# Kernel optimization log

Hardware: AMD Instinct MI355X
Metric: run time of the kernel (lower is better)

Reference implementation:

```python
import jax, jax.numpy as jnp
import numpy as np

D_MODEL = 1024
NUM_HEADS = 16
D_K = D_MODEL // NUM_HEADS
BATCH = 2
SEQ = 2048


def setup_inputs() -> dict:
    key = jax.random.key(0)
    ks = jax.random.split(key, 9)
    s = 1.0 / np.sqrt(D_MODEL)
    X = jax.random.normal(ks[0], (BATCH, SEQ, D_MODEL), dtype=jnp.float32)
    # causal mask, broadcastable over batch and heads; 0 means masked
    mask = jnp.tril(jnp.ones((SEQ, SEQ), dtype=jnp.int32))[None, None]
    W_Q = jax.random.uniform(ks[1], (D_MODEL, D_MODEL), jnp.float32, -s, s)
    b_Q = jax.random.uniform(ks[2], (D_MODEL,), jnp.float32, -s, s)
    W_K = jax.random.uniform(ks[3], (D_MODEL, D_MODEL), jnp.float32, -s, s)
    b_K = jax.random.uniform(ks[4], (D_MODEL,), jnp.float32, -s, s)
    W_V = jax.random.uniform(ks[5], (D_MODEL, D_MODEL), jnp.float32, -s, s)
    b_V = jax.random.uniform(ks[6], (D_MODEL,), jnp.float32, -s, s)
    W_O = jax.random.uniform(ks[7], (D_MODEL, D_MODEL), jnp.float32, -s, s)
    b_O = jax.random.uniform(ks[8], (D_MODEL,), jnp.float32, -s, s)
    return {"X": X, "mask": mask, "W_Q": W_Q, "b_Q": b_Q, "W_K": W_K,
            "b_K": b_K, "W_V": W_V, "b_V": b_V, "W_O": W_O, "b_O": b_O}


def reference(X, mask, W_Q, b_Q, W_K, b_K, W_V, b_V, W_O, b_O):
    B, S, _ = X.shape
    H, Dk = NUM_HEADS, D_K
    # projections; torch Linear uses y = x @ W.T + b; here W_* is stored as [in, out]
    Q = (X @ W_Q + b_Q).reshape(B, S, H, Dk).transpose(0, 2, 1, 3)  # [B,H,S,Dk]
    K = (X @ W_K + b_K).reshape(B, S, H, Dk).transpose(0, 2, 1, 3)
    V = (X @ W_V + b_V).reshape(B, S, H, Dk).transpose(0, 2, 1, 3)
    scores = jnp.einsum("bhqd,bhkd->bhqk", Q, K) / jnp.sqrt(jnp.asarray(Dk, X.dtype))
    scores = jnp.where(mask == 0, -jnp.inf, scores)
    attn = jax.nn.softmax(scores, axis=-1)  # [B,H,S,S]
    out = jnp.einsum("bhqk,bhkd->bhqd", attn, V)
    out = out.transpose(0, 2, 1, 3).reshape(B, S, H * Dk)
    return out @ W_O + b_O
```

## Files before the change

### kernel.cpp

```cpp
#include <hip/hip_runtime.h>
#include <math.h>

#define S_LEN 2048
#define DM 1024
#define NH 16
#define DK 64
#define BB 2
#define MROWS (BB * S_LEN)
#define QTILES (S_LEN / 64)
#define LOG2E 1.44269504088896340736f

typedef __attribute__((ext_vector_type(8))) short bf16x8;
typedef __attribute__((ext_vector_type(4))) float f32x4;

__device__ __forceinline__ unsigned short f2bf(float f) {
    unsigned int u = __builtin_bit_cast(unsigned int, f);
    u += 0x7fff + ((u >> 16) & 1);
    return (unsigned short)(u >> 16);
}

__device__ __forceinline__ float hw_exp2(float x) {
    return __builtin_amdgcn_exp2f(x);
}

__device__ __forceinline__ void gload_lds16(const unsigned short* g, unsigned short* l) {
    __builtin_amdgcn_global_load_lds(
        (const __attribute__((address_space(1))) unsigned int*)(const void*)g,
        (__attribute__((address_space(3))) unsigned int*)(void*)l, 16, 0, 0);
}

__global__ __launch_bounds__(256) void convert_bf16_kernel(
    const float* __restrict__ in, unsigned short* __restrict__ out, int n) {
    int i = (blockIdx.x * 256 + threadIdx.x) * 4;
    if (i + 3 < n) {
        float4 v = *(const float4*)(in + i);
        ushort4 o;
        o.x = f2bf(v.x); o.y = f2bf(v.y); o.z = f2bf(v.z); o.w = f2bf(v.w);
        *(ushort4*)(out + i) = o;
    }
}

__global__ __launch_bounds__(256) void transpose_bf16_kernel(
    const float* __restrict__ in, unsigned short* __restrict__ out,
    int rows, int cols) {
    __shared__ float tile[32][33];
    const int tx = threadIdx.x & 31, ty = threadIdx.x >> 5;
    const int c = blockIdx.x * 32 + tx;
    for (int i = 0; i < 32; i += 8)
        tile[ty + i][tx] = in[(size_t)(blockIdx.y * 32 + ty + i) * cols + c];
    __syncthreads();
    const int oc = blockIdx.y * 32 + tx;
    for (int i = 0; i < 32; i += 8)
        out[(size_t)(blockIdx.x * 32 + ty + i) * rows + oc] = f2bf(tile[tx][ty + i]);
}

__global__ __launch_bounds__(256) void gemm_bf16_kernel(
    const unsigned short* __restrict__ A,
    const unsigned short* __restrict__ Bt,
    const float* __restrict__ bQ, const float* __restrict__ bK,
    const float* __restrict__ bV,
    unsigned short* __restrict__ outQ, unsigned short* __restrict__ outK,
    unsigned short* __restrict__ outV,
    float* __restrict__ out_f,
    int K, int mode) {
    __shared__ __align__(16) unsigned short smem[4 * 64 * 72];
    const int tid = threadIdx.x;
    const int wave = tid >> 6, lane = tid & 63;
    const int lq = lane >> 4, ln = lane & 15;
    const int m0 = blockIdx.y * 128, n0 = blockIdx.x * 128;
    const int wr = (wave >> 1) * 64, wc = (wave & 1) * 64;

    f32x4 acc[4][4];
#pragma unroll
    for (int i = 0; i < 4; ++i)
#pragma unroll
        for (int j = 0; j < 4; ++j)
            acc[i][j] = (f32x4){0.f, 0.f, 0.f, 0.f};

    const unsigned short* ga = A  + (size_t)(m0 + (tid >> 2)) * K + (tid & 3) * 8;
    const unsigned short* gb = Bt + (size_t)(n0 + (tid >> 2)) * K + (tid & 3) * 8;
    const size_t half = (size_t)64 * K;

    {
        unsigned short* An = smem;
        unsigned short* Bn = smem + 4096;
        gload_lds16(ga, An + tid * 8);
        gload_lds16(ga + half, An + 2048 + tid * 8);
        gload_lds16(gb, Bn + tid * 8);
        gload_lds16(gb + half, Bn + 2048 + tid * 8);
    }

    for (int k0 = 0; k0 < K; k0 += 32) {
        const int cur = (k0 >> 5) & 1;
        unsigned short* As = smem + cur * 8192;
        unsigned short* Bs = As + 4096;
        __syncthreads();
        if (k0 + 32 < K) {
            unsigned short* An = smem + (cur ^ 1) * 8192;
            unsigned short* Bn = An + 4096;
            gload_lds16(ga + k0 + 32, An + tid * 8);
            gload_lds16(ga + half + k0 + 32, An + 2048 + tid * 8);
            gload_lds16(gb + k0 + 32, Bn + tid * 8);
            gload_lds16(gb + half + k0 + 32, Bn + 2048 + tid * 8);
        }
        bf16x8 af[4], bfv[4];
#pragma unroll
        for (int i = 0; i < 4; ++i) af[i]  = *(const bf16x8*)&As[(wr + i * 16 + ln) * 32 + lq * 8];
#pragma unroll
        for (int j = 0; j < 4; ++j) bfv[j] = *(const bf16x8*)&Bs[(wc + j * 16 + ln) * 32 + lq * 8];
#pragma unroll
        for (int i = 0; i < 4; ++i)
#pragma unroll
            for (int j = 0; j < 4; ++j)
                acc[i][j] = __builtin_amdgcn_mfma_f32_16x16x32_bf16(af[i], bfv[j], acc[i][j], 0, 0, 0);
    }
    __syncthreads();

    if (mode == 0) {
        const int which = n0 >> 10;
        const float* bias = which == 0 ? bQ : (which == 1 ? bK : bV);
        const float scale = which == 0 ? 0.125f * LOG2E : 1.0f;
        unsigned short* ob = which == 0 ? outQ : (which == 1 ? outK : outV);
        unsigned short* Ts = &smem[wave * 64 * 72];
#pragma unroll
        for (int i = 0; i < 4; ++i)
#pragma unroll
            for (int j = 0; j < 4; ++j)
#pragma unroll
                for (int r = 0; r < 4; ++r) {
                    int rl = i * 16 + lq * 4 + r;
                    int cl = j * 16 + ln;
                    float v = (acc[i][j][r] + bias[(n0 & 1023) + wc + cl]) * scale;
                    if (which == 2) Ts[cl * 72 + rl] = f2bf(v);
                    else            Ts[rl * 72 + cl] = f2bf(v);
                }
        const int hh = ((n0 & 1023) + wc) >> 6;
        const int bI = (m0 + wr) >> 11, sbase = (m0 + wr) & 2047;
        if (which <= 1) {
            unsigned short* dst = ob + ((size_t)(bI * NH + hh) * S_LEN + sbase) * DK;
#pragma unroll
            for (int t = 0; t < 8; ++t) {
                int rl = t * 8 + (lane >> 3);
                *(uint4*)(dst + rl * DK + (lane & 7) * 8) =
                    *(const uint4*)&Ts[rl * 72 + (lane & 7) * 8];
            }
        } else {
            unsigned short* dst = ob + ((size_t)(bI * NH + hh) * DK) * S_LEN + sbase;
#pragma unroll
            for (int t = 0; t < 8; ++t) {
                int dkl = t * 8 + (lane >> 3);
                *(uint4*)(dst + (size_t)dkl * S_LEN + (lane & 7) * 8) =
                    *(const uint4*)&Ts[dkl * 72 + (lane & 7) * 8];
            }
        }
    } else {
#pragma unroll
        for (int i = 0; i < 4; ++i)
#pragma unroll
            for (int j = 0; j < 4; ++j)
#pragma unroll
                for (int r = 0; r < 4; ++r) {
                    int m = m0 + wr + i * 16 + lq * 4 + r;
                    int n = n0 + wc + j * 16 + ln;
                    out_f[(size_t)m * DM + n] = acc[i][j][r] + bQ[n];
                }
    }
}

__global__ __launch_bounds__(256, 2) void attn_kernel(
    const unsigned short* __restrict__ Qg,
    const unsigned short* __restrict__ Kg,
    const unsigned short* __restrict__ Vg,
    unsigned short* __restrict__ Og) {
    __shared__ __align__(16) unsigned short KBUF[2 * 128 * 64];
    __shared__ __align__(16) unsigned short VBUF[2 * 64 * 128];
    __shared__ __align__(16) unsigned short Pw[4][16 * 40];

    const int tid = threadIdx.x;
    const int wave = tid >> 6, lane = tid & 63;
    const int lq = lane >> 4, ln = lane & 15;
    const int bh = blockIdx.y, b = bh >> 4, h = bh & 15;
    const int bx = blockIdx.x;
    const int qtA = QTILES - 1 - bx, qtB = bx;
    const int nkvA = (qtA + 2) >> 1;
    const int nkvB = (qtB + 2) >> 1;
    const int T = nkvA + nkvB;

    const unsigned short* Qb = Qg + (size_t)bh * S_LEN * DK;
    const unsigned short* Kb = Kg + (size_t)bh * S_LEN * DK;
    const unsigned short* Vb = Vg + (size_t)bh * DK * S_LEN;

    const int krow_l = lane >> 3;
    const int kchunk = (lane & 7) ^ krow_l;
    const int vrow_l = lane >> 4;

    {
#pragma unroll
        for (int s = 0; s < 4; ++s)
            gload_lds16(Kb + (size_t)(wave * 32 + s * 8 + krow_l) * DK + kchunk * 8,
                        KBUF + (wave * 32 + s * 8) * 64 + lane * 8);
#pragma unroll
        for (int s = 0; s < 4; ++s) {
            int rv = wave * 16 + s * 4 + vrow_l;
            int c  = (lane & 15) ^ (s * 4 + vrow_l);
            gload_lds16(Vb + (size_t)rv * S_LEN + c * 8,
                        VBUF + (wave * 16 + s * 4) * 128 + lane * 8);
        }
    }

    int q0 = qtA * 64;
    const int qrowoff = wave * 16 + ln;
    bf16x8 qf0 = *(const bf16x8*)(Qb + (q0 + qrowoff) * DK + lq * 8);
    bf16x8 qf1 = *(const bf16x8*)(Qb + (q0 + qrowoff) * DK + 32 + lq * 8);

    f32x4 oacc[4];
#pragma unroll
    for (int i = 0; i < 4; ++i) oacc[i] = (f32x4){0.f, 0.f, 0.f, 0.f};
    float m0r = -INFINITY, m1r = -INFINITY, m2r = -INFINITY, m3r = -INFINITY;
    float l0r = 0.f, l1r = 0.f, l2r = 0.f, l3r = 0.f;

    for (int g = 0; g < T; ++g) {
        const int cur = g & 1;
        unsigned short* Kl = KBUF + cur * 8192;
        unsigned short* Vl = VBUF + cur * 8192;
        __syncthreads();

        if (g + 1 < T) {
            const int kv0n = (g + 1 < nkvA ? g + 1 : g + 1 - nkvA) * 128;
            unsigned short* Kn = KBUF + (cur ^ 1) * 8192;
            unsigned short* Vn = VBUF + (cur ^ 1) * 8192;
#pragma unroll
            for (int s = 0; s < 4; ++s)
                gload_lds16(Kb + (size_t)(kv0n + wave * 32 + s * 8 + krow_l) * DK + kchunk * 8,
                            Kn + (wave * 32 + s * 8) * 64 + lane * 8);
#pragma unroll
            for (int s = 0; s < 4; ++s) {
                int rv = wave * 16 + s * 4 + vrow_l;
                int c  = (lane & 15) ^ (s * 4 + vrow_l);
                gload_lds16(Vb + (size_t)rv * S_LEN + kv0n + c * 8,
                            Vn + (wave * 16 + s * 4) * 128 + lane * 8);
            }
        }

        const int kv0 = (g < nkvA ? g : g - nkvA) * 128;
        const bool lastOfSeg = (g == nkvA - 1) || (g == T - 1);

        f32x4 sc[8];
#pragma unroll
        for (int ct = 0; ct < 8; ++ct) {
            const int rbase = (ct * 16 + ln) * 64;
            bf16x8 k0 = *(const bf16x8*)&Kl[rbase + ((lq ^ (ln & 7)) * 8)];
            bf16x8 k1 = *(const bf16x8*)&Kl[rbase + (((lq + 4) ^ (ln & 7)) * 8)];
            f32x4 a = (f32x4){0.f, 0.f, 0.f, 0.f};
            a = __builtin_amdgcn_mfma_f32_16x16x32_bf16(qf0, k0, a, 0, 0, 0);
            a = __builtin_amdgcn_mfma_f32_16x16x32_bf16(qf1, k1, a, 0, 0, 0);
            sc[ct] = a;
        }

        if (lastOfSeg) {
#pragma unroll
            for (int ct = 0; ct < 8; ++ct) {
                int col = kv0 + ct * 16 + ln;
#pragma unroll
                for (int r = 0; r < 4; ++r) {
                    int row = q0 + wave * 16 + lq * 4 + r;
                    if (col > row) sc[ct][r] = -INFINITY;
                }
            }
        }

#pragma unroll
        for (int r = 0; r < 4; ++r) {
            float mx = fmaxf(fmaxf(fmaxf(sc[0][r], sc[1][r]), fmaxf(sc[2][r], sc[3][r])),
                             fmaxf(fmaxf(sc[4][r], sc[5][r]), fmaxf(sc[6][r], sc[7][r])));
#pragma unroll
            for (int off = 1; off < 16; off <<= 1)
                mx = fmaxf(mx, __shfl_xor(mx, off));
            float mold = r == 0 ? m0r : (r == 1 ? m1r : (r == 2 ? m2r : m3r));
            float mnew = fmaxf(mold, mx);
            float alpha = hw_exp2(mold - mnew);
#pragma unroll
            for (int dkt = 0; dkt < 4; ++dkt) oacc[dkt][r] *= alpha;
            float rs = 0.f;
#pragma unroll
            for (int ct = 0; ct < 8; ++ct) {
                float pv = hw_exp2(sc[ct][r] - mnew);
                sc[ct][r] = pv;
                rs += pv;
            }
#pragma unroll
            for (int off = 1; off < 16; off <<= 1)
                rs += __shfl_xor(rs, off);
            if (r == 0) { l0r = l0r * alpha + rs; m0r = mnew; }
            else if (r == 1) { l1r = l1r * alpha + rs; m1r = mnew; }
            else if (r == 2) { l2r = l2r * alpha + rs; m2r = mnew; }
            else { l3r = l3r * alpha + rs; m3r = mnew; }
        }

        unsigned short* Pp = Pw[wave];
#pragma unroll
        for (int qd = 0; qd < 4; ++qd) {
#pragma unroll
            for (int c2 = 0; c2 < 2; ++c2)
#pragma unroll
                for (int r = 0; r < 4; ++r)
                    Pp[(lq * 4 + r) * 40 + c2 * 16 + ln] = f2bf(sc[qd * 2 + c2][r]);
            bf16x8 pf = *(const bf16x8*)&Pp[ln * 40 + lq * 8];
#pragma unroll
            for (int dkt = 0; dkt < 4; ++dkt) {
                const unsigned short* vr =
                    &Vl[(dkt * 16 + ln) * 128 + (((qd * 4 + lq) ^ ln) * 8)];
                oacc[dkt] = __builtin_amdgcn_mfma_f32_16x16x32_bf16(pf, *(const bf16x8*)vr, oacc[dkt], 0, 0, 0);
            }
        }

        if (g == nkvA - 1) {
#pragma unroll
            for (int r = 0; r < 4; ++r) {
                float lr = r == 0 ? l0r : (r == 1 ? l1r : (r == 2 ? l2r : l3r));
                float inv = 1.0f / lr;
                int s = q0 + wave * 16 + lq * 4 + r;
#pragma unroll
                for (int dkt = 0; dkt < 4; ++dkt)
                    Og[((size_t)(b * S_LEN + s)) * DM + h * 64 + dkt * 16 + ln] =
                        f2bf(oacc[dkt][r] * inv);
            }
            q0 = qtB * 64;
            qf0 = *(const bf16x8*)(Qb + (q0 + qrowoff) * DK + lq * 8);
            qf1 = *(const bf16x8*)(Qb + (q0 + qrowoff) * DK + 32 + lq * 8);
#pragma unroll
            for (int i = 0; i < 4; ++i) oacc[i] = (f32x4){0.f, 0.f, 0.f, 0.f};
            m0r = m1r = m2r = m3r = -INFINITY;
            l0r = l1r = l2r = l3r = 0.f;
        }
    }

#pragma unroll
    for (int r = 0; r < 4; ++r) {
        float lr = r == 0 ? l0r : (r == 1 ? l1r : (r == 2 ? l2r : l3r));
        float inv = 1.0f / lr;
        int s = q0 + wave * 16 + lq * 4 + r;
#pragma unroll
        for (int dkt = 0; dkt < 4; ++dkt)
            Og[((size_t)(b * S_LEN + s)) * DM + h * 64 + dkt * 16 + ln] =
                f2bf(oacc[dkt][r] * inv);
    }
}

extern "C" void kernel_launch(void* const* d_in, const int* in_sizes, int n_in,
                              void* d_out, int out_size, void* d_ws, size_t ws_size,
                              hipStream_t stream) {
    const float* X   = (const float*)d_in[0];
    const float* W_Q = (const float*)d_in[2];
    const float* b_Q = (const float*)d_in[3];
    const float* W_K = (const float*)d_in[4];
    const float* b_K = (const float*)d_in[5];
    const float* W_V = (const float*)d_in[6];
    const float* b_V = (const float*)d_in[7];
    const float* W_O = (const float*)d_in[8];
    const float* b_O = (const float*)d_in[9];

    unsigned short* Xb    = (unsigned short*)d_ws;
    unsigned short* WqkvT = Xb    + (size_t)MROWS * DM;
    unsigned short* WoT   = WqkvT + (size_t)3 * DM * DM;
    unsigned short* Qb    = WoT   + (size_t)DM * DM;
    unsigned short* Kb    = Qb    + (size_t)MROWS * DM;
    unsigned short* Vtb   = Kb    + (size_t)MROWS * DM;
    unsigned short* Ob    = Vtb   + (size_t)MROWS * DM;

    convert_bf16_kernel<<<(MROWS * DM) / 1024, 256, 0, stream>>>(X, Xb, MROWS * DM);
    dim3 tg(DM / 32, DM / 32);
    transpose_bf16_kernel<<<tg, 256, 0, stream>>>(W_Q, WqkvT, DM, DM);
    transpose_bf16_kernel<<<tg, 256, 0, stream>>>(W_K, WqkvT + (size_t)DM * DM, DM, DM);
    transpose_bf16_kernel<<<tg, 256, 0, stream>>>(W_V, WqkvT + (size_t)2 * DM * DM, DM, DM);
    transpose_bf16_kernel<<<tg, 256, 0, stream>>>(W_O, WoT, DM, DM);

    gemm_bf16_kernel<<<dim3(3 * DM / 128, MROWS / 128), 256, 0, stream>>>(
        Xb, WqkvT, b_Q, b_K, b_V, Qb, Kb, Vtb, nullptr, DM, 0);

    attn_kernel<<<dim3(QTILES / 2, BB * NH), 256, 0, stream>>>(Qb, Kb, Vtb, Ob);

    gemm_bf16_kernel<<<dim3(DM / 128, MROWS / 128), 256, 0, stream>>>(
        Ob, WoT, b_O, nullptr, nullptr, nullptr, nullptr, nullptr, (float*)d_out, DM, 1);
}
```

Before: 226.9 us.

## Merge prep kernels, add narrower O-projection GEMM, compute softmax row sums via MFMA

```diff
diff --git a/kernel.cpp b/kernel.cpp
--- a/kernel.cpp
+++ b/kernel.cpp
@@ -29,40 +29,45 @@
         (__attribute__((address_space(3))) unsigned int*)(void*)l, 16, 0, 0);
 }
 
-__global__ __launch_bounds__(256) void convert_bf16_kernel(
-    const float* __restrict__ in, unsigned short* __restrict__ out, int n) {
-    int i = (blockIdx.x * 256 + threadIdx.x) * 4;
-    if (i + 3 < n) {
-        float4 v = *(const float4*)(in + i);
+__global__ __launch_bounds__(256) void prep_kernel(
+    const float* __restrict__ X, unsigned short* __restrict__ Xb,
+    const float* __restrict__ W_Q, const float* __restrict__ W_K,
+    const float* __restrict__ W_V, const float* __restrict__ W_O,
+    unsigned short* __restrict__ WqkvT, unsigned short* __restrict__ WoT) {
+    const int z = blockIdx.z;
+    if (z == 0) {
+        int i = (blockIdx.x * 256 + threadIdx.x) * 4;
+        float4 v = *(const float4*)(X + i);
         ushort4 o;
         o.x = f2bf(v.x); o.y = f2bf(v.y); o.z = f2bf(v.z); o.w = f2bf(v.w);
-        *(ushort4*)(out + i) = o;
-    }
-}
-
-__global__ __launch_bounds__(256) void transpose_bf16_kernel(
-    const float* __restrict__ in, unsigned short* __restrict__ out,
-    int rows, int cols) {
+        *(ushort4*)(Xb + i) = o;
+        return;
+    }
+    if (blockIdx.x >= (DM / 32) * (DM / 32)) return;
+    const float* in = z == 1 ? W_Q : (z == 2 ? W_K : (z == 3 ? W_V : W_O));
+    unsigned short* out = z == 4 ? WoT : (WqkvT + (size_t)(z - 1) * DM * DM);
     __shared__ float tile[32][33];
+    const int bx = blockIdx.x & 31, by = blockIdx.x >> 5;
     const int tx = threadIdx.x & 31, ty = threadIdx.x >> 5;
-    const int c = blockIdx.x * 32 + tx;
+    const int c = bx * 32 + tx;
+#pragma unroll
     for (int i = 0; i < 32; i += 8)
-        tile[ty + i][tx] = in[(size_t)(blockIdx.y * 32 + ty + i) * cols + c];
+        tile[ty + i][tx] = in[(size_t)(by * 32 + ty + i) * DM + c];
     __syncthreads();
-    const int oc = blockIdx.y * 32 + tx;
+    const int oc = by * 32 + tx;
+#pragma unroll
     for (int i = 0; i < 32; i += 8)
-        out[(size_t)(blockIdx.x * 32 + ty + i) * rows + oc] = f2bf(tile[tx][ty + i]);
-}
-
-__global__ __launch_bounds__(256) void gemm_bf16_kernel(
+        out[(size_t)(bx * 32 + ty + i) * DM + oc] = f2bf(tile[tx][ty + i]);
+}
+
+__global__ __launch_bounds__(256) void gemm_qkv_kernel(
     const unsigned short* __restrict__ A,
     const unsigned short* __restrict__ Bt,
     const float* __restrict__ bQ, const float* __restrict__ bK,
     const float* __restrict__ bV,
     unsigned short* __restrict__ outQ, unsigned short* __restrict__ outK,
-    unsigned short* __restrict__ outV,
-    float* __restrict__ out_f,
-    int K, int mode) {
+    unsigned short* __restrict__ outV) {
+    const int K = DM;
     __shared__ __align__(16) unsigned short smem[4 * 64 * 72];
     const int tid = threadIdx.x;
     const int wave = tid >> 6, lane = tid & 63;
@@ -116,55 +121,108 @@
     }
     __syncthreads();
 
-    if (mode == 0) {
-        const int which = n0 >> 10;
-        const float* bias = which == 0 ? bQ : (which == 1 ? bK : bV);
-        const float scale = which == 0 ? 0.125f * LOG2E : 1.0f;
-        unsigned short* ob = which == 0 ? outQ : (which == 1 ? outK : outV);
-        unsigned short* Ts = &smem[wave * 64 * 72];
+    const int which = n0 >> 10;
+    const float* bias = which == 0 ? bQ : (which == 1 ? bK : bV);
+    const float scale = which == 0 ? 0.125f * LOG2E : 1.0f;
+    unsigned short* ob = which == 0 ? outQ : (which == 1 ? outK : outV);
+    unsigned short* Ts = &smem[wave * 64 * 72];
+#pragma unroll
+    for (int i = 0; i < 4; ++i)
+#pragma unroll
+        for (int j = 0; j < 4; ++j)
+#pragma unroll
+            for (int r = 0; r < 4; ++r) {
+                int rl = i * 16 + lq * 4 + r;
+                int cl = j * 16 + ln;
+                float v = (acc[i][j][r] + bias[(n0 & 1023) + wc + cl]) * scale;
+                if (which == 2) Ts[cl * 72 + rl] = f2bf(v);
+                else            Ts[rl * 72 + cl] = f2bf(v);
+            }
+    const int hh = ((n0 & 1023) + wc) >> 6;
+    const int bI = (m0 + wr) >> 11, sbase = (m0 + wr) & 2047;
+    if (which <= 1) {
+        unsigned short* dst = ob + ((size_t)(bI * NH + hh) * S_LEN + sbase) * DK;
+#pragma unroll
+        for (int t = 0; t < 8; ++t) {
+            int rl = t * 8 + (lane >> 3);
+            *(uint4*)(dst + rl * DK + (lane & 7) * 8) =
+                *(const uint4*)&Ts[rl * 72 + (lane & 7) * 8];
+        }
+    } else {
+        unsigned short* dst = ob + ((size_t)(bI * NH + hh) * DK) * S_LEN + sbase;
+#pragma unroll
+        for (int t = 0; t < 8; ++t) {
+            int dkl = t * 8 + (lane >> 3);
+            *(uint4*)(dst + (size_t)dkl * S_LEN + (lane & 7) * 8) =
+                *(const uint4*)&Ts[dkl * 72 + (lane & 7) * 8];
+        }
+    }
+}
+
+__global__ __launch_bounds__(256) void gemm_o_kernel(
+    const unsigned short* __restrict__ A,
+    const unsigned short* __restrict__ Bt,
+    const float* __restrict__ bias,
+    float* __restrict__ out_f) {
+    const int K = DM;
+    __shared__ __align__(16) unsigned short smem[2 * 6144];
+    const int tid = threadIdx.x;
+    const int wave = tid >> 6, lane = tid & 63;
+    const int lq = lane >> 4, ln = lane & 15;
+    const int m0 = blockIdx.y * 128, n0 = blockIdx.x * 64;
+    const int wr = (wave >> 1) * 64, wc = (wave & 1) * 32;
+
+    f32x4 acc[4][2];
+#pragma unroll
+    for (int i = 0; i < 4; ++i)
+#pragma unroll
+        for (int j = 0; j < 2; ++j)
+            acc[i][j] = (f32x4){0.f, 0.f, 0.f, 0.f};
+
+    const unsigned short* ga = A  + (size_t)(m0 + (tid >> 2)) * K + (tid & 3) * 8;
+    const unsigned short* gb = Bt + (size_t)(n0 + (tid >> 2)) * K + (tid & 3) * 8;
+    const size_t half = (size_t)64 * K;
+
+    {
+        unsigned short* An = smem;
+        gload_lds16(ga, An + tid * 8);
+        gload_lds16(ga + half, An + 2048 + tid * 8);
+        gload_lds16(gb, An + 4096 + tid * 8);
+    }
+
+    for (int k0 = 0; k0 < K; k0 += 32) {
+        const int cur = (k0 >> 5) & 1;
+        unsigned short* As = smem + cur * 6144;
+        unsigned short* Bs = As + 4096;
+        __syncthreads();
+        if (k0 + 32 < K) {
+            unsigned short* An = smem + (cur ^ 1) * 6144;
+            gload_lds16(ga + k0 + 32, An + tid * 8);
+            gload_lds16(ga + half + k0 + 32, An + 2048 + tid * 8);
+            gload_lds16(gb + k0 + 32, An + 4096 + tid * 8);
+        }
+        bf16x8 af[4], bfv[2];
+#pragma unroll
+        for (int i = 0; i < 4; ++i) af[i]  = *(const bf16x8*)&As[(wr + i * 16 + ln) * 32 + lq * 8];
+#pragma unroll
+        for (int j = 0; j < 2; ++j) bfv[j] = *(const bf16x8*)&Bs[(wc + j * 16 + ln) * 32 + lq * 8];
 #pragma unroll
         for (int i = 0; i < 4; ++i)
 #pragma unroll
-            for (int j = 0; j < 4; ++j)
-#pragma unroll
-                for (int r = 0; r < 4; ++r) {
-                    int rl = i * 16 + lq * 4 + r;
-                    int cl = j * 16 + ln;
-                    float v = (acc[i][j][r] + bias[(n0 & 1023) + wc + cl]) * scale;
-                    if (which == 2) Ts[cl * 72 + rl] = f2bf(v);
-                    else            Ts[rl * 72 + cl] = f2bf(v);
-                }
-        const int hh = ((n0 & 1023) + wc) >> 6;
-        const int bI = (m0 + wr) >> 11, sbase = (m0 + wr) & 2047;
-        if (which <= 1) {
-            unsigned short* dst = ob + ((size_t)(bI * NH + hh) * S_LEN + sbase) * DK;
-#pragma unroll
-            for (int t = 0; t < 8; ++t) {
-                int rl = t * 8 + (lane >> 3);
-                *(uint4*)(dst + rl * DK + (lane & 7) * 8) =
-                    *(const uint4*)&Ts[rl * 72 + (lane & 7) * 8];
-            }
-        } else {
-            unsigned short* dst = ob + ((size_t)(bI * NH + hh) * DK) * S_LEN + sbase;
-#pragma unroll
-            for (int t = 0; t < 8; ++t) {
-                int dkl = t * 8 + (lane >> 3);
-                *(uint4*)(dst + (size_t)dkl * S_LEN + (lane & 7) * 8) =
-                    *(const uint4*)&Ts[dkl * 72 + (lane & 7) * 8];
-            }
-        }
-    } else {
-#pragma unroll
-        for (int i = 0; i < 4; ++i)
-#pragma unroll
-            for (int j = 0; j < 4; ++j)
-#pragma unroll
-                for (int r = 0; r < 4; ++r) {
-                    int m = m0 + wr + i * 16 + lq * 4 + r;
-                    int n = n0 + wc + j * 16 + ln;
-                    out_f[(size_t)m * DM + n] = acc[i][j][r] + bQ[n];
-                }
-    }
+            for (int j = 0; j < 2; ++j)
+                acc[i][j] = __builtin_amdgcn_mfma_f32_16x16x32_bf16(af[i], bfv[j], acc[i][j], 0, 0, 0);
+    }
+
+#pragma unroll
+    for (int i = 0; i < 4; ++i)
+#pragma unroll
+        for (int j = 0; j < 2; ++j)
+#pragma unroll
+            for (int r = 0; r < 4; ++r) {
+                int m = m0 + wr + i * 16 + lq * 4 + r;
+                int n = n0 + wc + j * 16 + ln;
+                out_f[(size_t)m * DM + n] = acc[i][j][r] + bias[n];
+            }
 }
 
 __global__ __launch_bounds__(256, 2) void attn_kernel(
@@ -213,11 +271,15 @@
     bf16x8 qf0 = *(const bf16x8*)(Qb + (q0 + qrowoff) * DK + lq * 8);
     bf16x8 qf1 = *(const bf16x8*)(Qb + (q0 + qrowoff) * DK + 32 + lq * 8);
 
+    const short one_bf = (short)0x3F80;
+    const bf16x8 onesf = {one_bf, one_bf, one_bf, one_bf,
+                          one_bf, one_bf, one_bf, one_bf};
+
     f32x4 oacc[4];
+    f32x4 lacc = (f32x4){0.f, 0.f, 0.f, 0.f};
 #pragma unroll
     for (int i = 0; i < 4; ++i) oacc[i] = (f32x4){0.f, 0.f, 0.f, 0.f};
     float m0r = -INFINITY, m1r = -INFINITY, m2r = -INFINITY, m3r = -INFINITY;
-    float l0r = 0.f, l1r = 0.f, l2r = 0.f, l3r = 0.f;
 
     for (int g = 0; g < T; ++g) {
         const int cur = g & 1;
@@ -281,20 +343,14 @@
             float alpha = hw_exp2(mold - mnew);
 #pragma unroll
             for (int dkt = 0; dkt < 4; ++dkt) oacc[dkt][r] *= alpha;
-            float rs = 0.f;
-#pragma unroll
-            for (int ct = 0; ct < 8; ++ct) {
-                float pv = hw_exp2(sc[ct][r] - mnew);
-                sc[ct][r] = pv;
-                rs += pv;
-            }
-#pragma unroll
-            for (int off = 1; off < 16; off <<= 1)
-                rs += __shfl_xor(rs, off);
-            if (r == 0) { l0r = l0r * alpha + rs; m0r = mnew; }
-            else if (r == 1) { l1r = l1r * alpha + rs; m1r = mnew; }
-            else if (r == 2) { l2r = l2r * alpha + rs; m2r = mnew; }
-            else { l3r = l3r * alpha + rs; m3r = mnew; }
+            lacc[r] *= alpha;
+#pragma unroll
+            for (int ct = 0; ct < 8; ++ct)
+                sc[ct][r] = hw_exp2(sc[ct][r] - mnew);
+            if (r == 0) m0r = mnew;
+            else if (r == 1) m1r = mnew;
+            else if (r == 2) m2r = mnew;
+            else m3r = mnew;
         }
 
         unsigned short* Pp = Pw[wave];
@@ -306,6 +362,7 @@
                 for (int r = 0; r < 4; ++r)
                     Pp[(lq * 4 + r) * 40 + c2 * 16 + ln] = f2bf(sc[qd * 2 + c2][r]);
             bf16x8 pf = *(const bf16x8*)&Pp[ln * 40 + lq * 8];
+            lacc = __builtin_amdgcn_mfma_f32_16x16x32_bf16(pf, onesf, lacc, 0, 0, 0);
 #pragma unroll
             for (int dkt = 0; dkt < 4; ++dkt) {
                 const unsigned short* vr =
@@ -317,8 +374,7 @@
         if (g == nkvA - 1) {
 #pragma unroll
             for (int r = 0; r < 4; ++r) {
-                float lr = r == 0 ? l0r : (r == 1 ? l1r : (r == 2 ? l2r : l3r));
-                float inv = 1.0f / lr;
+                float inv = 1.0f / lacc[r];
                 int s = q0 + wave * 16 + lq * 4 + r;
 #pragma unroll
                 for (int dkt = 0; dkt < 4; ++dkt)
@@ -330,15 +386,14 @@
             qf1 = *(const bf16x8*)(Qb + (q0 + qrowoff) * DK + 32 + lq * 8);
 #pragma unroll
             for (int i = 0; i < 4; ++i) oacc[i] = (f32x4){0.f, 0.f, 0.f, 0.f};
+            lacc = (f32x4){0.f, 0.f, 0.f, 0.f};
             m0r = m1r = m2r = m3r = -INFINITY;
-            l0r = l1r = l2r = l3r = 0.f;
         }
     }
 
 #pragma unroll
     for (int r = 0; r < 4; ++r) {
-        float lr = r == 0 ? l0r : (r == 1 ? l1r : (r == 2 ? l2r : l3r));
-        float inv = 1.0f / lr;
+        float inv = 1.0f / lacc[r];
         int s = q0 + wave * 16 + lq * 4 + r;
 #pragma unroll
         for (int dkt = 0; dkt < 4; ++dkt)
@@ -368,18 +423,14 @@
     unsigned short* Vtb   = Kb    + (size_t)MROWS * DM;
     unsigned short* Ob    = Vtb   + (size_t)MROWS * DM;
 
-    convert_bf16_kernel<<<(MROWS * DM) / 1024, 256, 0, stream>>>(X, Xb, MROWS * DM);
-    dim3 tg(DM / 32, DM / 32);
-    transpose_bf16_kernel<<<tg, 256, 0, stream>>>(W_Q, WqkvT, DM, DM);
-    transpose_bf16_kernel<<<tg, 256, 0, stream>>>(W_K, WqkvT + (size_t)DM * DM, DM, DM);
-    transpose_bf16_kernel<<<tg, 256, 0, stream>>>(W_V, WqkvT + (size_t)2 * DM * DM, DM, DM);
-    transpose_bf16_kernel<<<tg, 256, 0, stream>>>(W_O, WoT, DM, DM);
-
-    gemm_bf16_kernel<<<dim3(3 * DM / 128, MROWS / 128), 256, 0, stream>>>(
-        Xb, WqkvT, b_Q, b_K, b_V, Qb, Kb, Vtb, nullptr, DM, 0);
+    prep_kernel<<<dim3((MROWS * DM) / 1024, 1, 5), 256, 0, stream>>>(
+        X, Xb, W_Q, W_K, W_V, W_O, WqkvT, WoT);
+
+    gemm_qkv_kernel<<<dim3(3 * DM / 128, MROWS / 128), 256, 0, stream>>>(
+        Xb, WqkvT, b_Q, b_K, b_V, Qb, Kb, Vtb);
 
     attn_kernel<<<dim3(QTILES / 2, BB * NH), 256, 0, stream>>>(Qb, Kb, Vtb, Ob);
 
-    gemm_bf16_kernel<<<dim3(DM / 128, MROWS / 128), 256, 0, stream>>>(
-        Ob, WoT, b_O, nullptr, nullptr, nullptr, nullptr, nullptr, (float*)d_out, DM, 1);
-}
+    gemm_o_kernel<<<dim3(DM / 64, MROWS / 128), 256, 0, stream>>>(
+        Ob, WoT, b_O, (float*)d_out);
+}
```

Result: faster. 203.6 us (-10.3%).
